# Performance work log

Measured on AMD Instinct MI355X. Metric: run time of the kernel, lower is better.

The kernel has to match this reference:

```python
import jax, jax.numpy as jnp
import numpy as np

EMBED_DIM = 1024
NUM_HEADS = 16
HEAD_DIM = EMBED_DIM // NUM_HEADS
N, SEQ = 4, 2048


def setup_inputs() -> dict:
    key = jax.random.key(0)
    ks = jax.random.split(key, 9)
    s = 0.02
    return {
        "keys": jax.random.normal(ks[0], (N, SEQ, EMBED_DIM), jnp.float32),
        "values": jax.random.normal(ks[1], (N, SEQ, EMBED_DIM), jnp.float32),
        "queries": jax.random.normal(ks[2], (N, SEQ, EMBED_DIM), jnp.float32),
        "mask": jax.random.randint(ks[3], (N, 1, SEQ, SEQ), 0, 2, jnp.int32),
        "Wk": jax.random.normal(ks[4], (HEAD_DIM, HEAD_DIM), jnp.float32) * s,
        "Wv": jax.random.normal(ks[5], (HEAD_DIM, HEAD_DIM), jnp.float32) * s,
        "Wq": jax.random.normal(ks[6], (HEAD_DIM, HEAD_DIM), jnp.float32) * s,
        "Wo": jax.random.normal(ks[7], (EMBED_DIM, EMBED_DIM), jnp.float32) * s,
        "bo": jax.random.normal(ks[8], (EMBED_DIM,), jnp.float32) * s,
    }


def reference(keys, values, queries, mask, Wk, Wv, Wq, Wo, bo):
    n, key_len, _ = keys.shape
    value_len = values.shape[1]
    query_len = queries.shape[1]
    # Faithful to source: direct reshape (N, L, E) -> (N, H, L, D), no transpose.
    k = keys.reshape(n, NUM_HEADS, key_len, HEAD_DIM) @ Wk.T
    v = values.reshape(n, NUM_HEADS, value_len, HEAD_DIM) @ Wv.T
    q = queries.reshape(n, NUM_HEADS, query_len, HEAD_DIM) @ Wq.T
    # Scaled by sqrt(embed_dim) as in the original (not sqrt(head_dim)).
    energy = jnp.einsum('nhqd,nhkd->nhqk', q, k) / jnp.sqrt(jnp.float32(EMBED_DIM))
    energy = jnp.where(mask == 0, jnp.float32(-1e20), energy)
    attention = jax.nn.softmax(energy, axis=-1)
    att_out = jnp.einsum('nhql,nhld->nhqd', attention, v)
    att_out = att_out.reshape(n, query_len, NUM_HEADS * HEAD_DIM)
    return att_out @ Wo.T + bo
```

## Files before the change

### kernel.cpp

```cpp
#include <hip/hip_runtime.h>

#define SEQ 2048
#define HDIM 64
#define NH 16

typedef __bf16 bf16x8 __attribute__((ext_vector_type(8)));
typedef float f32x4 __attribute__((ext_vector_type(4)));
typedef unsigned short u16x8 __attribute__((ext_vector_type(8)));
typedef unsigned short u16x4 __attribute__((ext_vector_type(4)));
typedef _Float16 f16x4 __attribute__((ext_vector_type(4)));
typedef unsigned int u32x2 __attribute__((ext_vector_type(2)));
typedef unsigned long long u64;

__device__ __forceinline__ unsigned short f2bf(float f) {
  unsigned int u = __builtin_bit_cast(unsigned int, f);
  u = (u + 0x7FFFu + ((u >> 16) & 1u)) >> 16;
  return (unsigned short)u;
}

__device__ __forceinline__ bf16x8 cvt8(f32x4 a, f32x4 b) {
  u16x8 u;
  u[0] = f2bf(a[0]); u[1] = f2bf(a[1]); u[2] = f2bf(a[2]); u[3] = f2bf(a[3]);
  u[4] = f2bf(b[0]); u[5] = f2bf(b[1]); u[6] = f2bf(b[2]); u[7] = f2bf(b[3]);
  return __builtin_bit_cast(bf16x8, u);
}

__device__ __forceinline__ f32x4 mfma16(bf16x8 a, bf16x8 b, f32x4 c) {
  return __builtin_amdgcn_mfma_f32_16x16x32_bf16(a, b, c, 0, 0, 0);
}
__device__ __forceinline__ f32x4 mfma16h(f16x4 a, f16x4 b, f32x4 c) {
  return __builtin_amdgcn_mfma_f32_16x16x16f16(a, b, c, 0, 0, 0);
}

__device__ __forceinline__ f16x4 pk4h(float a, float b, float cc, float d) {
  auto h0 = __builtin_amdgcn_cvt_pkrtz(a, b);
  auto h1 = __builtin_amdgcn_cvt_pkrtz(cc, d);
  u32x2 u = { __builtin_bit_cast(unsigned int, h0),
              __builtin_bit_cast(unsigned int, h1) };
  return __builtin_bit_cast(f16x4, u);
}

#define QSCALE 0.045084220027780106f

__global__ __launch_bounds__(256) void qkv_proj(
    const float* __restrict__ keys, const float* __restrict__ values,
    const float* __restrict__ queries,
    const float* __restrict__ Wk, const float* __restrict__ Wv,
    const float* __restrict__ Wq,
    unsigned short* __restrict__ kb, unsigned short* __restrict__ vb,
    unsigned short* __restrict__ qb)
{
  const int which = blockIdx.y;
  const float* __restrict__ in = (which == 0) ? keys : (which == 1) ? values : queries;
  const float* __restrict__ W  = (which == 0) ? Wk   : (which == 1) ? Wv     : Wq;
  unsigned short* __restrict__ op = (which == 0) ? kb : (which == 1) ? vb : qb;
  const float osc = (which == 2) ? QSCALE : 1.0f;
  const bool asf16 = (which == 1);

  const int tid = threadIdx.x;
  const int w = tid >> 6, lane = tid & 63, c = lane & 15, quad = lane >> 4;

  bf16x8 aw[4][2];
  #pragma unroll
  for (int dt = 0; dt < 4; ++dt)
    #pragma unroll
    for (int hh = 0; hh < 2; ++hh) {
      const float* wr = W + (dt * 16 + c) * 64 + hh * 32 + quad * 8;
      aw[dt][hh] = cvt8(*(const f32x4*)wr, *(const f32x4*)(wr + 4));
    }

  const int m00 = blockIdx.x * 256 + w * 64;
  #pragma unroll
  for (int s = 0; s < 4; ++s) {
    const int m0 = m00 + s * 16;
    const float* xr = in + (size_t)(m0 + c) * 64;
    bf16x8 x0 = cvt8(*(const f32x4*)(xr + quad * 8), *(const f32x4*)(xr + quad * 8 + 4));
    bf16x8 x1 = cvt8(*(const f32x4*)(xr + 32 + quad * 8), *(const f32x4*)(xr + 36 + quad * 8));
    f32x4 acc[4] = {};
    #pragma unroll
    for (int dt = 0; dt < 4; ++dt) {
      acc[dt] = mfma16(aw[dt][0], x0, acc[dt]);
      acc[dt] = mfma16(aw[dt][1], x1, acc[dt]);
    }
    unsigned short* orow = op + (size_t)(m0 + c) * 64 + quad * 4;
    #pragma unroll
    for (int dt = 0; dt < 4; ++dt) {
      u16x4 pk;
      if (asf16) {
        pk = __builtin_bit_cast(u16x4,
            pk4h(acc[dt][0], acc[dt][1], acc[dt][2], acc[dt][3]));
      } else {
        pk[0] = f2bf(acc[dt][0] * osc); pk[1] = f2bf(acc[dt][1] * osc);
        pk[2] = f2bf(acc[dt][2] * osc); pk[3] = f2bf(acc[dt][3] * osc);
      }
      *(u16x4*)(orow + dt * 16) = pk;
    }
  }
}

__global__ __launch_bounds__(256) void cvt_wo(const float* __restrict__ src,
                                              unsigned short* __restrict__ dst)
{
  int i = (blockIdx.x * 256 + threadIdx.x) * 4;
  f32x4 v = *reinterpret_cast<const f32x4*>(src + i);
  u16x4 o;
  o[0] = f2bf(v[0]); o[1] = f2bf(v[1]); o[2] = f2bf(v[2]); o[3] = f2bf(v[3]);
  *reinterpret_cast<u16x4*>(dst + i) = o;
}

__global__ __launch_bounds__(256) void maskpack(const int* __restrict__ mask,
                                                u64* __restrict__ bits)
{
  const int wid = blockIdx.x * 4 + (threadIdx.x >> 6);
  const int lane = threadIdx.x & 63;
  const int* src = mask + (size_t)wid * 1024 + lane;
  u64* dst = bits + (size_t)wid * 16;
  #pragma unroll
  for (int i = 0; i < 16; ++i) {
    u64 b = __ballot(src[i * 64] != 0);
    if (lane == 0) dst[i] = b;
  }
}

__global__ __launch_bounds__(256, 4) void attn4(
    const unsigned short* __restrict__ qb, const unsigned short* __restrict__ kb,
    const unsigned short* __restrict__ vb, const u64* __restrict__ mbits,
    unsigned short* __restrict__ att)
{
  __shared__ __attribute__((aligned(16))) unsigned short Kl[64][72];
  __shared__ __attribute__((aligned(16))) unsigned short Vt[64][76];
  __shared__ unsigned int mlut[16][2];

  const int tid = threadIdx.x;
  const int w = tid >> 6, lane = tid & 63, c = lane & 15, quad = lane >> 4;
  const int h = blockIdx.y, n = blockIdx.z;
  const int q0 = blockIdx.x * 128;
  const size_t hb = (size_t)(n * NH + h) * (SEQ * HDIM);

  if (tid < 16) {
    unsigned m = tid;
    mlut[m][0] = ((m & 1u) ? 0xFFFFu : 0u) | ((m & 2u) ? 0xFFFF0000u : 0u);
    mlut[m][1] = ((m & 4u) ? 0xFFFFu : 0u) | ((m & 8u) ? 0xFFFF0000u : 0u);
  }

  bf16x8 aq[2][2];
  #pragma unroll
  for (int qt = 0; qt < 2; ++qt) {
    const unsigned short* qr = qb + hb + (size_t)(q0 + qt * 64 + w * 16 + c) * HDIM;
    aq[qt][0] = *reinterpret_cast<const bf16x8*>(qr + quad * 8);
    aq[qt][1] = *reinterpret_cast<const bf16x8*>(qr + 32 + quad * 8);
  }

  f32x4 o[2][4] = {};
  f32x4 osum[2] = {};
  const f16x4 ones = {(_Float16)1.f, (_Float16)1.f, (_Float16)1.f, (_Float16)1.f};

  const u64* mb = mbits + ((size_t)n * SEQ + q0 + w * 16 + c) * 32;

  const bool isK = tid < 128;
  const int krow = tid >> 1, kcol = (tid & 1) * 32;
  const int vg = (tid >> 3) & 15, vd8 = tid & 7;

  const unsigned short* kptr = kb + hb + (size_t)krow * HDIM + kcol;
  const unsigned short* vptr = vb + hb + (size_t)(vg * 4) * HDIM + vd8 * 8;

  u16x8 st0, st1, st2, st3;
  if (isK) {
    st0 = *(const u16x8*)(kptr);
    st1 = *(const u16x8*)(kptr + 8);
    st2 = *(const u16x8*)(kptr + 16);
    st3 = *(const u16x8*)(kptr + 24);
  } else {
    st0 = *(const u16x8*)(vptr);
    st1 = *(const u16x8*)(vptr + HDIM);
    st2 = *(const u16x8*)(vptr + 2 * HDIM);
    st3 = *(const u16x8*)(vptr + 3 * HDIM);
  }

  for (int step = 0; step < 32; ++step) {
    __syncthreads();
    if (isK) {
      *(u16x8*)&Kl[krow][kcol]      = st0;
      *(u16x8*)&Kl[krow][kcol + 8]  = st1;
      *(u16x8*)&Kl[krow][kcol + 16] = st2;
      *(u16x8*)&Kl[krow][kcol + 24] = st3;
    } else {
      #pragma unroll
      for (int j = 0; j < 8; ++j) {
        u16x4 pk = { st0[j], st1[j], st2[j], st3[j] };
        *(u16x4*)&Vt[vd8 * 8 + j][vg * 4] = pk;
      }
    }
    if (step < 31) {
      const size_t adv = (size_t)(step + 1) * 64 * HDIM;
      if (isK) {
        st0 = *(const u16x8*)(kptr + adv);
        st1 = *(const u16x8*)(kptr + adv + 8);
        st2 = *(const u16x8*)(kptr + adv + 16);
        st3 = *(const u16x8*)(kptr + adv + 24);
      } else {
        st0 = *(const u16x8*)(vptr + adv);
        st1 = *(const u16x8*)(vptr + adv + HDIM);
        st2 = *(const u16x8*)(vptr + adv + 2 * HDIM);
        st3 = *(const u16x8*)(vptr + adv + 3 * HDIM);
      }
    }
    __syncthreads();

    f32x4 e[2][4] = {};
    #pragma unroll
    for (int t = 0; t < 4; ++t) {
      bf16x8 kf0 = *reinterpret_cast<const bf16x8*>(&Kl[t * 16 + c][quad * 8]);
      bf16x8 kf1 = *reinterpret_cast<const bf16x8*>(&Kl[t * 16 + c][32 + quad * 8]);
      #pragma unroll
      for (int qt = 0; qt < 2; ++qt) {
        e[qt][t] = mfma16(kf0, aq[qt][0], e[qt][t]);
        e[qt][t] = mfma16(kf1, aq[qt][1], e[qt][t]);
      }
    }

    u64 b0 = mb[step] >> (quad * 4);
    u64 b1 = mb[2048 + step] >> (quad * 4);

    f16x4 pf[2][4];
    #pragma unroll
    for (int qt = 0; qt < 2; ++qt) {
      u64 bb = qt ? b1 : b0;
      unsigned int lo = (unsigned int)bb, hi = (unsigned int)(bb >> 32);
      #pragma unroll
      for (int t = 0; t < 4; ++t) {
        unsigned int nib = (((t & 2) ? hi : lo) >> ((t & 1) * 16)) & 0xFu;
        f32x4 ev = e[qt][t];
        f16x4 pk = pk4h(exp2f(ev[0]), exp2f(ev[1]), exp2f(ev[2]), exp2f(ev[3]));
        u32x2 pw = __builtin_bit_cast(u32x2, pk);
        pw[0] &= mlut[nib][0];
        pw[1] &= mlut[nib][1];
        pf[qt][t] = __builtin_bit_cast(f16x4, pw);
      }
    }

    #pragma unroll
    for (int dt = 0; dt < 4; ++dt) {
      #pragma unroll
      for (int t = 0; t < 4; ++t) {
        f16x4 vf = __builtin_bit_cast(f16x4,
            *(const u16x4*)&Vt[dt * 16 + c][t * 16 + quad * 4]);
        o[0][dt] = mfma16h(vf, pf[0][t], o[0][dt]);
        o[1][dt] = mfma16h(vf, pf[1][t], o[1][dt]);
      }
    }
    #pragma unroll
    for (int t = 0; t < 4; ++t) {
      osum[0] = mfma16h(ones, pf[0][t], osum[0]);
      osum[1] = mfma16h(ones, pf[1][t], osum[1]);
    }
  }

  #pragma unroll
  for (int qt = 0; qt < 2; ++qt) {
    float inv = 1.0f / osum[qt][0];
    unsigned short* orow =
        att + hb + (size_t)(q0 + qt * 64 + w * 16 + c) * HDIM + quad * 4;
    #pragma unroll
    for (int dt = 0; dt < 4; ++dt) {
      u16x4 pk = { f2bf(o[qt][dt][0] * inv), f2bf(o[qt][dt][1] * inv),
                   f2bf(o[qt][dt][2] * inv), f2bf(o[qt][dt][3] * inv) };
      *(u16x4*)(orow + dt * 16) = pk;
    }
  }
}

__global__ __launch_bounds__(256) void out_proj3(
    const unsigned short* __restrict__ att, const unsigned short* __restrict__ wob,
    const float* __restrict__ bo, float* __restrict__ out)
{
  __shared__ __attribute__((aligned(16))) unsigned short As[64][72];
  __shared__ __attribute__((aligned(16))) unsigned short Bs[128][72];

  const int nb = blockIdx.x, mbk = blockIdx.y;
  const int tid = threadIdx.x;
  const int w = tid >> 6, lane = tid & 63, c = lane & 15, quad = lane >> 4;
  const int wm = w & 1, wn = w >> 1;
  const int m0 = mbk * 64, n0 = nb * 128;
  const int arow = tid >> 2, acol = (tid & 3) * 16;
  const int brow = tid >> 1, bcol = (tid & 1) * 32;

  f32x4 acc[2][4] = {};

  for (int k0 = 0; k0 < 1024; k0 += 64) {
    __syncthreads();
    {
      const unsigned short* sa = att + (size_t)(m0 + arow) * 1024 + k0 + acol;
      const unsigned short* sb = wob + (size_t)(n0 + brow) * 1024 + k0 + bcol;
      *(u16x8*)&As[arow][acol]     = *(const u16x8*)(sa);
      *(u16x8*)&As[arow][acol + 8] = *(const u16x8*)(sa + 8);
      #pragma unroll
      for (int i = 0; i < 4; ++i)
        *(u16x8*)&Bs[brow][bcol + i * 8] = *(const u16x8*)(sb + i * 8);
    }
    __syncthreads();

    #pragma unroll
    for (int kk = 0; kk < 64; kk += 32) {
      bf16x8 af[2];
      #pragma unroll
      for (int mt = 0; mt < 2; ++mt)
        af[mt] = *reinterpret_cast<const bf16x8*>(&As[wm * 32 + mt * 16 + c][kk + quad * 8]);
      #pragma unroll
      for (int nt = 0; nt < 4; ++nt) {
        bf16x8 bf_ = *reinterpret_cast<const bf16x8*>(&Bs[wn * 64 + nt * 16 + c][kk + quad * 8]);
        #pragma unroll
        for (int mt = 0; mt < 2; ++mt)
          acc[mt][nt] = mfma16(af[mt], bf_, acc[mt][nt]);
      }
    }
  }

  #pragma unroll
  for (int nt = 0; nt < 4; ++nt) {
    const int col = n0 + wn * 64 + nt * 16 + c;
    const float bias = bo[col];
    #pragma unroll
    for (int mt = 0; mt < 2; ++mt)
      #pragma unroll
      for (int r = 0; r < 4; ++r)
        out[(size_t)(m0 + wm * 32 + mt * 16 + quad * 4 + r) * 1024 + col] =
            acc[mt][nt][r] + bias;
  }
}

extern "C" void kernel_launch(void* const* d_in, const int* in_sizes, int n_in,
                              void* d_out, int out_size, void* d_ws, size_t ws_size,
                              hipStream_t stream) {
  const float* keys    = (const float*)d_in[0];
  const float* values  = (const float*)d_in[1];
  const float* queries = (const float*)d_in[2];
  const int*   mask    = (const int*)d_in[3];
  const float* Wk      = (const float*)d_in[4];
  const float* Wv      = (const float*)d_in[5];
  const float* Wq      = (const float*)d_in[6];
  const float* Wo      = (const float*)d_in[7];
  const float* bo      = (const float*)d_in[8];
  float* out = (float*)d_out;

  const size_t T = (size_t)4 * NH * SEQ * HDIM;
  unsigned short* ws  = (unsigned short*)d_ws;
  unsigned short* kb  = ws;
  unsigned short* vb  = kb + T;
  unsigned short* qb  = vb + T;
  unsigned short* att = qb + T;
  unsigned short* wob = att + T;
  u64* mbits = (u64*)(wob + 1024 * 1024);

  qkv_proj<<<dim3(512, 3), 256, 0, stream>>>(keys, values, queries,
                                             Wk, Wv, Wq, kb, vb, qb);
  cvt_wo<<<dim3(1024), 256, 0, stream>>>(Wo, wob);
  maskpack<<<dim3(4096), 256, 0, stream>>>(mask, mbits);
  attn4<<<dim3(16, NH, 4), 256, 0, stream>>>(qb, kb, vb, mbits, att);
  out_proj3<<<dim3(8, 128), 256, 0, stream>>>(att, wob, bo, out);
}
```

Baseline: 373.4 us.

## Write V transposed in projection and remap attention blocks across XCDs

The QKV projection now stores V (the f16 path) transposed as [head][d][seq], so the attention kernel can fill its LDS V tile with plain vector stores instead of an in-register transpose, and the Vt padding is reduced. The attention grid is flattened to 1D and remapped so that blocks on the same XCD share the same (batch, head), improving L2 reuse of K/V. The transposed V write uses scalar 2-byte strided global stores, which may cost more in the projection kernel.

Result: no change. 369.4 us (-1.1%).

```diff
diff --git a/kernel.cpp b/kernel.cpp
--- a/kernel.cpp
+++ b/kernel.cpp
@@ -82,18 +82,26 @@
       acc[dt] = mfma16(aw[dt][0], x0, acc[dt]);
       acc[dt] = mfma16(aw[dt][1], x1, acc[dt]);
     }
-    unsigned short* orow = op + (size_t)(m0 + c) * 64 + quad * 4;
-    #pragma unroll
-    for (int dt = 0; dt < 4; ++dt) {
-      u16x4 pk;
-      if (asf16) {
-        pk = __builtin_bit_cast(u16x4,
+    if (asf16) {
+      unsigned short* vt = op + (size_t)(m0 >> 11) * (64 * SEQ)
+                              + ((m0 & 2047) + c);
+      #pragma unroll
+      for (int dt = 0; dt < 4; ++dt) {
+        u16x4 pk = __builtin_bit_cast(u16x4,
             pk4h(acc[dt][0], acc[dt][1], acc[dt][2], acc[dt][3]));
-      } else {
+        #pragma unroll
+        for (int r = 0; r < 4; ++r)
+          vt[(size_t)(dt * 16 + quad * 4 + r) * SEQ] = pk[r];
+      }
+    } else {
+      unsigned short* orow = op + (size_t)(m0 + c) * 64 + quad * 4;
+      #pragma unroll
+      for (int dt = 0; dt < 4; ++dt) {
+        u16x4 pk;
         pk[0] = f2bf(acc[dt][0] * osc); pk[1] = f2bf(acc[dt][1] * osc);
         pk[2] = f2bf(acc[dt][2] * osc); pk[3] = f2bf(acc[dt][3] * osc);
-      }
-      *(u16x4*)(orow + dt * 16) = pk;
+        *(u16x4*)(orow + dt * 16) = pk;
+      }
     }
   }
 }
@@ -128,14 +136,19 @@
     unsigned short* __restrict__ att)
 {
   __shared__ __attribute__((aligned(16))) unsigned short Kl[64][72];
-  __shared__ __attribute__((aligned(16))) unsigned short Vt[64][76];
+  __shared__ __attribute__((aligned(16))) unsigned short Vt[64][72];
   __shared__ unsigned int mlut[16][2];
 
   const int tid = threadIdx.x;
   const int w = tid >> 6, lane = tid & 63, c = lane & 15, quad = lane >> 4;
-  const int h = blockIdx.y, n = blockIdx.z;
-  const int q0 = blockIdx.x * 128;
-  const size_t hb = (size_t)(n * NH + h) * (SEQ * HDIM);
+
+  const int bid = blockIdx.x;
+  const int xcd = bid & 7, rr = bid >> 3;
+  const int qx = rr & 15, gh = rr >> 4;
+  const int G = xcd + gh * 8;
+  const int n = G >> 4;
+  const int q0 = qx * 128;
+  const size_t hb = (size_t)G * (SEQ * HDIM);
 
   if (tid < 16) {
     unsigned m = tid;
@@ -158,52 +171,29 @@
   const u64* mb = mbits + ((size_t)n * SEQ + q0 + w * 16 + c) * 32;
 
   const bool isK = tid < 128;
-  const int krow = tid >> 1, kcol = (tid & 1) * 32;
-  const int vg = (tid >> 3) & 15, vd8 = tid & 7;
-
-  const unsigned short* kptr = kb + hb + (size_t)krow * HDIM + kcol;
-  const unsigned short* vptr = vb + hb + (size_t)(vg * 4) * HDIM + vd8 * 8;
-
-  u16x8 st0, st1, st2, st3;
-  if (isK) {
-    st0 = *(const u16x8*)(kptr);
-    st1 = *(const u16x8*)(kptr + 8);
-    st2 = *(const u16x8*)(kptr + 16);
-    st3 = *(const u16x8*)(kptr + 24);
-  } else {
-    st0 = *(const u16x8*)(vptr);
-    st1 = *(const u16x8*)(vptr + HDIM);
-    st2 = *(const u16x8*)(vptr + 2 * HDIM);
-    st3 = *(const u16x8*)(vptr + 3 * HDIM);
-  }
+  const int srow = (tid & 127) >> 1, scol = (tid & 1) * 32;
+  const unsigned short* sptr = (isK ? kb : vb) + hb
+      + (size_t)srow * (isK ? HDIM : SEQ) + scol;
+  const int sadv = isK ? 64 * HDIM : 64;
+  unsigned short (*Sl)[72] = isK ? Kl : Vt;
+
+  u16x8 st0 = *(const u16x8*)(sptr);
+  u16x8 st1 = *(const u16x8*)(sptr + 8);
+  u16x8 st2 = *(const u16x8*)(sptr + 16);
+  u16x8 st3 = *(const u16x8*)(sptr + 24);
 
   for (int step = 0; step < 32; ++step) {
     __syncthreads();
-    if (isK) {
-      *(u16x8*)&Kl[krow][kcol]      = st0;
-      *(u16x8*)&Kl[krow][kcol + 8]  = st1;
-      *(u16x8*)&Kl[krow][kcol + 16] = st2;
-      *(u16x8*)&Kl[krow][kcol + 24] = st3;
-    } else {
-      #pragma unroll
-      for (int j = 0; j < 8; ++j) {
-        u16x4 pk = { st0[j], st1[j], st2[j], st3[j] };
-        *(u16x4*)&Vt[vd8 * 8 + j][vg * 4] = pk;
-      }
-    }
+    *(u16x8*)&Sl[srow][scol]      = st0;
+    *(u16x8*)&Sl[srow][scol + 8]  = st1;
+    *(u16x8*)&Sl[srow][scol + 16] = st2;
+    *(u16x8*)&Sl[srow][scol + 24] = st3;
     if (step < 31) {
-      const size_t adv = (size_t)(step + 1) * 64 * HDIM;
-      if (isK) {
-        st0 = *(const u16x8*)(kptr + adv);
-        st1 = *(const u16x8*)(kptr + adv + 8);
-        st2 = *(const u16x8*)(kptr + adv + 16);
-        st3 = *(const u16x8*)(kptr + adv + 24);
-      } else {
-        st0 = *(const u16x8*)(vptr + adv);
-        st1 = *(const u16x8*)(vptr + adv + HDIM);
-        st2 = *(const u16x8*)(vptr + adv + 2 * HDIM);
-        st3 = *(const u16x8*)(vptr + adv + 3 * HDIM);
-      }
+      const unsigned short* p = sptr + (size_t)(step + 1) * sadv;
+      st0 = *(const u16x8*)(p);
+      st1 = *(const u16x8*)(p + 8);
+      st2 = *(const u16x8*)(p + 16);
+      st3 = *(const u16x8*)(p + 24);
     }
     __syncthreads();
 
@@ -356,6 +346,6 @@
                                              Wk, Wv, Wq, kb, vb, qb);
   cvt_wo<<<dim3(1024), 256, 0, stream>>>(Wo, wob);
   maskpack<<<dim3(4096), 256, 0, stream>>>(mask, mbits);
-  attn4<<<dim3(16, NH, 4), 256, 0, stream>>>(qb, kb, vb, mbits, att);
+  attn4<<<dim3(1024), 256, 0, stream>>>(qb, kb, vb, mbits, att);
   out_proj3<<<dim3(8, 128), 256, 0, stream>>>(att, wob, bo, out);
 }
```
